# Kernel optimization log

Measured on AMD Instinct MI355X. Metric: run time of the kernel, lower is better.

Reference implementation:

```python
import jax, jax.numpy as jnp
import numpy as np

B, VL, TL, KL = 2, 2048, 448, 64  # batch, vision_len, text_len, task_len
H, NH, D = 1024, 16, 64           # hidden, num_heads, head_dim


def _linear(x, w, b):
    # torch nn.Linear convention: w is [out, in]
    return x @ w.T + b


def _attn(q, k, v):
    # q: [b, ql, n, d], k/v: [b, kl, n, d] -> [b, ql, n, d]
    d = q.shape[-1]
    scores = jnp.einsum('bqnd,bknd->bnqk', q, k) / d  # note: /d, not /sqrt(d), as in source
    probs = jax.nn.softmax(scores, axis=-1)
    return jnp.einsum('bnqk,bknd->bqnd', probs, v)


def setup_inputs() -> dict:
    key = jax.random.key(0)
    ks = jax.random.split(key, 20)
    s = 0.02
    inp = {
        'vision_hidden_states': jax.random.normal(ks[0], (B, VL, H), jnp.float32),
        'text_hidden_states': jax.random.normal(ks[1], (B, TL, H), jnp.float32),
        'task_hidden_states': jax.random.normal(ks[2], (B, KL, H), jnp.float32),
        'wq0': jax.random.normal(ks[3], (H, H), jnp.float32) * s,
        'bq0': jnp.zeros((H,), jnp.float32),
        'wk0': jax.random.normal(ks[4], (H, H), jnp.float32) * s,
        'bk0': jnp.zeros((H,), jnp.float32),
        'wv0': jax.random.normal(ks[5], (H, H), jnp.float32) * s,
        'bv0': jnp.zeros((H,), jnp.float32),
        'wq1': jax.random.normal(ks[6], (D, D), jnp.float32) * s,
        'bq1': jnp.zeros((D,), jnp.float32),
        'wk1': jax.random.normal(ks[7], (D, D), jnp.float32) * s,
        'bk1': jnp.zeros((D,), jnp.float32),
        'wv1': jax.random.normal(ks[8], (D, D), jnp.float32) * s,
        'bv1': jnp.zeros((D,), jnp.float32),
        'wo': jax.random.normal(ks[9], (H, H), jnp.float32) * s,
        'bo': jnp.zeros((H,), jnp.float32),
    }
    return inp


def reference(vision_hidden_states, text_hidden_states, task_hidden_states,
              wq0, bq0, wk0, bk0, wv0, bv0,
              wq1, bq1, wk1, bk1, wv1, bv1, wo, bo):
    b, vl, h = vision_hidden_states.shape
    tl = text_hidden_states.shape[1]
    kl = task_hidden_states.shape[1]
    total = vl + tl + kl

    hs = jnp.concatenate([vision_hidden_states, text_hidden_states, task_hidden_states], axis=1)
    q0 = _linear(hs, wq0, bq0).reshape(b, total, NH, D)
    k0 = _linear(hs, wk0, bk0).reshape(b, total, NH, D)
    v0 = _linear(hs, wv0, bv0).reshape(b, total, NH, D)

    vq, tq, kq = q0[:, :vl], q0[:, vl:vl + tl], q0[:, vl + tl:]
    vk, tk, kk = k0[:, :vl], k0[:, vl:vl + tl], k0[:, vl + tl:]
    vv, tv = v0[:, :vl], v0[:, vl:vl + tl]
    kv = q0[:, vl + tl:]  # faithful to source bug: task_v comes from q0

    v2t = _attn(vq, tk, tv)  # vision attends to text: [b, vl, n, d]
    t2v = _attn(tq, vk, vv)  # text attends to vision: [b, tl, n, d]
    mid = jnp.concatenate([v2t, t2v], axis=1)  # [b, vl+tl, n, d]

    q1 = jnp.concatenate([kq, _linear(mid, wq1, bq1)], axis=1)
    k1 = jnp.concatenate([kk, _linear(mid, wk1, bk1)], axis=1)
    v1 = jnp.concatenate([kv, _linear(mid, wv1, bv1)], axis=1)

    out = _attn(q1, k1, v1).reshape(b, total, NH * D)
    return _linear(out, wo, bo)
```

## Files before the change

kernel.cpp:

```cpp
#include <hip/hip_runtime.h>
#include <math.h>

#define NB   2
#define VL   2048
#define TL   448
#define KL   64
#define TOT  2560
#define MIDL 2496
#define HDIM 1024
#define NHEAD 16
#define DHEAD 64

typedef __bf16 bf16x8 __attribute__((ext_vector_type(8)));
typedef float  f32x4  __attribute__((ext_vector_type(4)));
typedef unsigned short us8 __attribute__((ext_vector_type(8)));
typedef float  fl4    __attribute__((ext_vector_type(4)));
typedef unsigned int u32x2 __attribute__((ext_vector_type(2)));

__device__ __forceinline__ unsigned short f2bf(float f) {
    unsigned int u = __builtin_bit_cast(unsigned int, f);
    u += 0x7FFFu + ((u >> 16) & 1u);
    return (unsigned short)(u >> 16);
}
__device__ __forceinline__ f32x4 mfma_bf16(bf16x8 a, bf16x8 b, f32x4 c) {
    return __builtin_amdgcn_mfma_f32_16x16x32_bf16(a, b, c, 0, 0, 0);
}
__device__ __forceinline__ bf16x8 ldb(const unsigned short* p) {
    return __builtin_bit_cast(bf16x8, *(const us8*)p);
}
__device__ __forceinline__ unsigned cvt_pk_bf16(float lo, float hi) {
    unsigned r;
    asm("v_cvt_pk_bf16_f32 %0, %1, %2" : "=v"(r) : "v"(lo), "v"(hi));
    return r;
}
__device__ __forceinline__ float exp2_fast(float x) {
    float r;
    asm("v_exp_f32 %0, %1" : "=v"(r) : "v"(x));
    return r;
}

__global__ __launch_bounds__(256) void k_cast_hs(
    const float* __restrict__ vis, const float* __restrict__ txt,
    const float* __restrict__ tsk, unsigned short* __restrict__ X)
{
    size_t idx = ((size_t)blockIdx.x * 256 + threadIdx.x) * 4;
    if (idx >= (size_t)NB * TOT * HDIM) return;
    size_t r = idx >> 10; int c = (int)(idx & 1023);
    int b = (int)(r / TOT), s = (int)(r % TOT);
    const float* src;
    if (s < VL)        src = vis + ((size_t)b * VL + s) * HDIM;
    else if (s < MIDL) src = txt + ((size_t)b * TL + (s - VL)) * HDIM;
    else               src = tsk + ((size_t)b * KL + (s - MIDL)) * HDIM;
    fl4 v = *(const fl4*)(src + c);
    X[idx + 0] = f2bf(v[0]); X[idx + 1] = f2bf(v[1]);
    X[idx + 2] = f2bf(v[2]); X[idx + 3] = f2bf(v[3]);
}

__global__ __launch_bounds__(256) void k_cast(
    const float* __restrict__ in, unsigned short* __restrict__ out, int n)
{
    int idx = (blockIdx.x * 256 + threadIdx.x) * 4;
    if (idx >= n) return;
    fl4 v = *(const fl4*)(in + idx);
    out[idx + 0] = f2bf(v[0]); out[idx + 1] = f2bf(v[1]);
    out[idx + 2] = f2bf(v[2]); out[idx + 3] = f2bf(v[3]);
}

template<bool BF16OUT>
__global__ __launch_bounds__(256) void k_gemm_bt(
    const unsigned short* __restrict__ A, const unsigned short* __restrict__ W,
    const float* __restrict__ bias, void* __restrict__ Cv,
    int M, int N, int K)
{
    __shared__ unsigned short As[128][40];
    __shared__ unsigned short Bs[128][40];
    const int row0 = blockIdx.x * 128, col0 = blockIdx.y * 128;
    const int t = threadIdx.x;
    const int lane = t & 63, wave = t >> 6;
    const int wr = wave >> 1, wc = wave & 1;
    const int lrow = lane & 15, lgrp = lane >> 4;

    f32x4 acc[4][4];
    #pragma unroll
    for (int m = 0; m < 4; ++m)
        #pragma unroll
        for (int n = 0; n < 4; ++n)
            acc[m][n] = (f32x4){0.f, 0.f, 0.f, 0.f};

    const int r = t >> 1, hc = (t & 1) * 16;
    const unsigned short* Ap = A + (size_t)(row0 + r) * K + hc;
    const unsigned short* Wp = W + (size_t)(col0 + r) * K + hc;

    for (int kk = 0; kk < K; kk += 32) {
        us8 a0 = *(const us8*)(Ap + kk);
        us8 a1 = *(const us8*)(Ap + kk + 8);
        us8 b0 = *(const us8*)(Wp + kk);
        us8 b1 = *(const us8*)(Wp + kk + 8);
        __syncthreads();
        *(us8*)&As[r][hc]     = a0;
        *(us8*)&As[r][hc + 8] = a1;
        *(us8*)&Bs[r][hc]     = b0;
        *(us8*)&Bs[r][hc + 8] = b1;
        __syncthreads();
        bf16x8 af[4], bfr[4];
        #pragma unroll
        for (int m = 0; m < 4; ++m) af[m]  = ldb(&As[wr*64 + m*16 + lrow][lgrp*8]);
        #pragma unroll
        for (int n = 0; n < 4; ++n) bfr[n] = ldb(&Bs[wc*64 + n*16 + lrow][lgrp*8]);
        #pragma unroll
        for (int m = 0; m < 4; ++m)
            #pragma unroll
            for (int n = 0; n < 4; ++n)
                acc[m][n] = mfma_bf16(af[m], bfr[n], acc[m][n]);
    }
    #pragma unroll
    for (int m = 0; m < 4; ++m) {
        #pragma unroll
        for (int n = 0; n < 4; ++n) {
            int col = col0 + wc*64 + n*16 + lrow;
            float bs = bias[col];
            #pragma unroll
            for (int q = 0; q < 4; ++q) {
                int row = row0 + wr*64 + m*16 + lgrp*4 + q;
                float v = acc[m][n][q] + bs;
                if (BF16OUT) ((unsigned short*)Cv)[(size_t)row * N + col] = f2bf(v);
                else         ((float*)Cv)[(size_t)row * N + col] = v;
            }
        }
    }
}

__global__ __launch_bounds__(256) void k_gemm_qkv(
    const unsigned short* __restrict__ A, const unsigned short* __restrict__ W,
    const float* __restrict__ b0, const float* __restrict__ b1,
    const float* __restrict__ b2,
    unsigned short* __restrict__ C0, unsigned short* __restrict__ C1,
    unsigned short* __restrict__ vT)
{
    __shared__ unsigned short As[128][40];
    __shared__ unsigned short Bs[128][40];
    const int row0 = blockIdx.x * 128, col0 = blockIdx.y * 128;
    const int t = threadIdx.x;
    const int lane = t & 63, wave = t >> 6;
    const int wr = wave >> 1, wc = wave & 1;
    const int lrow = lane & 15, lgrp = lane >> 4;

    f32x4 acc[4][4];
    #pragma unroll
    for (int m = 0; m < 4; ++m)
        #pragma unroll
        for (int n = 0; n < 4; ++n)
            acc[m][n] = (f32x4){0.f, 0.f, 0.f, 0.f};

    const int r = t >> 1, hc = (t & 1) * 16;
    const unsigned short* Ap = A + (size_t)(row0 + r) * HDIM + hc;
    const unsigned short* Wp = W + (size_t)(col0 + r) * HDIM + hc;

    for (int kk = 0; kk < HDIM; kk += 32) {
        us8 a0 = *(const us8*)(Ap + kk);
        us8 a1 = *(const us8*)(Ap + kk + 8);
        us8 b0v = *(const us8*)(Wp + kk);
        us8 b1v = *(const us8*)(Wp + kk + 8);
        __syncthreads();
        *(us8*)&As[r][hc]     = a0;
        *(us8*)&As[r][hc + 8] = a1;
        *(us8*)&Bs[r][hc]     = b0v;
        *(us8*)&Bs[r][hc + 8] = b1v;
        __syncthreads();
        bf16x8 af[4], bfr[4];
        #pragma unroll
        for (int m = 0; m < 4; ++m) af[m]  = ldb(&As[wr*64 + m*16 + lrow][lgrp*8]);
        #pragma unroll
        for (int n = 0; n < 4; ++n) bfr[n] = ldb(&Bs[wc*64 + n*16 + lrow][lgrp*8]);
        #pragma unroll
        for (int m = 0; m < 4; ++m)
            #pragma unroll
            for (int n = 0; n < 4; ++n)
                acc[m][n] = mfma_bf16(af[m], bfr[n], acc[m][n]);
    }
    const int plane = col0 >> 10;
    const int cl0 = col0 & 1023;
    if (plane < 2) {
        const float* bp = (plane == 0) ? b0 : b1;
        unsigned short* Cp = (plane == 0) ? C0 : C1;
        #pragma unroll
        for (int m = 0; m < 4; ++m)
            #pragma unroll
            for (int n = 0; n < 4; ++n) {
                int col = cl0 + wc*64 + n*16 + lrow;
                float bs = bp[col];
                #pragma unroll
                for (int q = 0; q < 4; ++q) {
                    int row = row0 + wr*64 + m*16 + lgrp*4 + q;
                    Cp[(size_t)row * HDIM + col] = f2bf(acc[m][n][q] + bs);
                }
            }
    } else {
        #pragma unroll
        for (int m = 0; m < 4; ++m)
            #pragma unroll
            for (int n = 0; n < 4; ++n) {
                int col = cl0 + wc*64 + n*16 + lrow;
                int hh = col >> 6, dd = col & 63;
                float bs = b2[col];
                int rowb = row0 + wr*64 + m*16 + lgrp*4;
                int bb = rowb / TOT, sq = rowb % TOT;
                u32x2 w;
                w[0] = cvt_pk_bf16(acc[m][n][0] + bs, acc[m][n][1] + bs);
                w[1] = cvt_pk_bf16(acc[m][n][2] + bs, acc[m][n][3] + bs);
                *(u32x2*)(vT + ((size_t)(bb*NHEAD + hh)*64 + dd)*TOT + sq) = w;
            }
    }
}

__global__ __launch_bounds__(256) void k_attn(
    const unsigned short* __restrict__ Qb, const unsigned short* __restrict__ Kb,
    const unsigned short* __restrict__ vT, unsigned short* __restrict__ Ob,
    int Lk, size_t q_bs, size_t k_bs, int v_seq0, size_t o_bs, float scale)
{
    __shared__ unsigned short QV[64 * 72];
    __shared__ unsigned short Ks[64][72];
    __shared__ unsigned short Pl[4][16][72];

    const int b = blockIdx.z, h = blockIdx.y, qb = blockIdx.x;
    const unsigned short* Q = Qb + (size_t)b * q_bs + h * 64;
    const unsigned short* K = Kb + (size_t)b * k_bs + h * 64;
    const unsigned short* V = vT + ((size_t)(b*NHEAD + h) * 64) * TOT + v_seq0;
    unsigned short*       O = Ob + (size_t)b * o_bs + h * 64;
    const int t = threadIdx.x;
    const int wave = t >> 6, lane = t & 63;
    const int lrow = lane & 15, lgrp = lane >> 4;
    const int q0r = qb * 64;

    #pragma unroll
    for (int i = 0; i < 2; ++i) {
        int c = t + i * 256, rr = c >> 3, off = (c & 7) * 8;
        *(us8*)&QV[rr*72 + off] = *(const us8*)(Q + (size_t)(q0r + rr) * HDIM + off);
    }
    __syncthreads();
    bf16x8 qf0 = ldb(&QV[(wave*16 + lrow)*72 + lgrp*8]);
    bf16x8 qf1 = ldb(&QV[(wave*16 + lrow)*72 + 32 + lgrp*8]);

    f32x4 oacc[4];
    #pragma unroll
    for (int d = 0; d < 4; ++d) oacc[d] = (f32x4){0.f, 0.f, 0.f, 0.f};
    float mr = -INFINITY;
    float lsum = 0.f;

    const int c0 = t,        rr0 = c0 >> 3, of0 = (c0 & 7) * 8;
    const int c1 = t + 256,  rr1 = c1 >> 3, of1 = (c1 & 7) * 8;
    const unsigned short* Kp0 = K + (size_t)rr0 * HDIM + of0;
    const unsigned short* Kp1 = K + (size_t)rr1 * HDIM + of1;
    const unsigned short* Vp0 = V + (size_t)rr0 * TOT + of0;
    const unsigned short* Vp1 = V + (size_t)rr1 * TOT + of1;

    const int nkt = Lk >> 6;
    us8 ka0 = *(const us8*)(Kp0);
    us8 ka1 = *(const us8*)(Kp1);
    us8 va0 = *(const us8*)(Vp0);
    us8 va1 = *(const us8*)(Vp1);

    for (int kt = 0; kt < nkt; ++kt) {
        __syncthreads();
        *(us8*)&Ks[rr0][of0] = ka0;
        *(us8*)&Ks[rr1][of1] = ka1;
        *(us8*)&QV[rr0*72 + of0] = va0;
        *(us8*)&QV[rr1*72 + of1] = va1;
        if (kt + 1 < nkt) {
            ka0 = *(const us8*)(Kp0 + (size_t)(kt+1) * 64 * HDIM);
            ka1 = *(const us8*)(Kp1 + (size_t)(kt+1) * 64 * HDIM);
            va0 = *(const us8*)(Vp0 + (kt+1) * 64);
            va1 = *(const us8*)(Vp1 + (kt+1) * 64);
        }
        __syncthreads();

        f32x4 s[4];
        #pragma unroll
        for (int nf = 0; nf < 4; ++nf) {
            bf16x8 kf0 = ldb(&Ks[nf*16 + lrow][lgrp*8]);
            bf16x8 kf1 = ldb(&Ks[nf*16 + lrow][32 + lgrp*8]);
            f32x4 z = (f32x4){0.f, 0.f, 0.f, 0.f};
            z = mfma_bf16(kf0, qf0, z);
            z = mfma_bf16(kf1, qf1, z);
            s[nf] = z * scale;
        }
        float mt = s[0][0];
        #pragma unroll
        for (int nf = 0; nf < 4; ++nf)
            #pragma unroll
            for (int rg = 0; rg < 4; ++rg)
                mt = fmaxf(mt, s[nf][rg]);
        mt = fmaxf(mt, __shfl_xor(mt, 16));
        mt = fmaxf(mt, __shfl_xor(mt, 32));
        if (!__all(mt <= mr + 8.f)) {
            float mnew = fmaxf(mr, mt);
            float al = exp2_fast(mr - mnew);
            mr = mnew;
            lsum *= al;
            #pragma unroll
            for (int d = 0; d < 4; ++d) oacc[d] *= al;
        }

        float rs = 0.f;
        #pragma unroll
        for (int nf = 0; nf < 4; ++nf) {
            float p0 = exp2_fast(s[nf][0] - mr);
            float p1 = exp2_fast(s[nf][1] - mr);
            float p2 = exp2_fast(s[nf][2] - mr);
            float p3 = exp2_fast(s[nf][3] - mr);
            rs += (p0 + p1) + (p2 + p3);
            u32x2 w;
            w[0] = cvt_pk_bf16(p0, p1);
            w[1] = cvt_pk_bf16(p2, p3);
            *(u32x2*)&Pl[wave][lrow][nf*16 + lgrp*4] = w;
        }
        rs += __shfl_xor(rs, 16);
        rs += __shfl_xor(rs, 32);
        lsum += rs;

        bf16x8 pb0 = ldb(&Pl[wave][lrow][lgrp*8]);
        bf16x8 pb1 = ldb(&Pl[wave][lrow][32 + lgrp*8]);
        #pragma unroll
        for (int df = 0; df < 4; ++df) {
            int d = df*16 + lrow;
            bf16x8 v0 = ldb(&QV[d*72 + lgrp*8]);
            bf16x8 v1 = ldb(&QV[d*72 + 32 + lgrp*8]);
            oacc[df] = mfma_bf16(v0, pb0, oacc[df]);
            oacc[df] = mfma_bf16(v1, pb1, oacc[df]);
        }
    }
    const float rcp = 1.0f / lsum;
    const int row = q0r + wave*16 + lrow;
    #pragma unroll
    for (int df = 0; df < 4; ++df) {
        u32x2 w;
        w[0] = cvt_pk_bf16(oacc[df][0] * rcp, oacc[df][1] * rcp);
        w[1] = cvt_pk_bf16(oacc[df][2] * rcp, oacc[df][3] * rcp);
        *(u32x2*)(O + (size_t)row * HDIM + df*16 + lgrp*4) = w;
    }
}

__global__ __launch_bounds__(256) void k_midlin(
    const unsigned short* __restrict__ mid,
    const unsigned short* __restrict__ wq, const unsigned short* __restrict__ wk,
    const unsigned short* __restrict__ wv,
    const float* __restrict__ bq, const float* __restrict__ bk,
    const float* __restrict__ bv,
    unsigned short* __restrict__ q1, unsigned short* __restrict__ k1,
    unsigned short* __restrict__ vT)
{
    __shared__ unsigned short As[128][72];
    const int r0 = blockIdx.x * 128, h = blockIdx.y;
    const int t = threadIdx.x;
    const int wave = t >> 6, lane = t & 63;
    const int lrow = lane & 15, lgrp = lane >> 4;

    #pragma unroll
    for (int i = 0; i < 4; ++i) {
        int c = t + i * 256, rr = c >> 3, off = (c & 7) * 8;
        *(us8*)&As[rr][off] = *(const us8*)(mid + (size_t)(r0 + rr) * HDIM + h*64 + off);
    }
    __syncthreads();
    bf16x8 af[2][2];
    #pragma unroll
    for (int m = 0; m < 2; ++m)
        #pragma unroll
        for (int kf = 0; kf < 2; ++kf)
            af[m][kf] = ldb(&As[wave*32 + m*16 + lrow][kf*32 + lgrp*8]);

    const unsigned short* ws[3] = {wq, wk, wv};
    const float* bs[3] = {bq, bk, bv};
    unsigned short* ds[2] = {q1, k1};
    #pragma unroll
    for (int o = 0; o < 3; ++o) {
        bf16x8 bfr[4][2];
        #pragma unroll
        for (int n = 0; n < 4; ++n)
            #pragma unroll
            for (int kf = 0; kf < 2; ++kf)
                bfr[n][kf] = __builtin_bit_cast(bf16x8,
                    *(const us8*)(ws[o] + (size_t)(n*16 + lrow) * 64 + kf*32 + lgrp*8));
        f32x4 acc[2][4];
        #pragma unroll
        for (int m = 0; m < 2; ++m)
            #pragma unroll
            for (int n = 0; n < 4; ++n) {
                f32x4 z = (f32x4){0.f, 0.f, 0.f, 0.f};
                z = mfma_bf16(af[m][0], bfr[n][0], z);
                z = mfma_bf16(af[m][1], bfr[n][1], z);
                acc[m][n] = z;
            }
        #pragma unroll
        for (int m = 0; m < 2; ++m)
            #pragma unroll
            for (int n = 0; n < 4; ++n) {
                float bb = bs[o][n*16 + lrow];
                if (o < 2) {
                    #pragma unroll
                    for (int q = 0; q < 4; ++q) {
                        int gr = r0 + wave*32 + m*16 + lgrp*4 + q;
                        int bi = gr / MIDL, sq = gr % MIDL;
                        size_t drow = (size_t)bi * TOT + 64 + sq;
                        ds[o][drow * HDIM + h*64 + n*16 + lrow] = f2bf(acc[m][n][q] + bb);
                    }
                } else {
                    int gr = r0 + wave*32 + m*16 + lgrp*4;
                    int bi = gr / MIDL, sq = gr % MIDL;
                    u32x2 w;
                    w[0] = cvt_pk_bf16(acc[m][n][0] + bb, acc[m][n][1] + bb);
                    w[1] = cvt_pk_bf16(acc[m][n][2] + bb, acc[m][n][3] + bb);
                    *(u32x2*)(vT + ((size_t)(bi*NHEAD + h)*64 + (n*16+lrow))*TOT
                              + 64 + sq) = w;
                }
            }
    }
}

__global__ __launch_bounds__(256) void k_copy_task(
    const unsigned short* __restrict__ q0, const unsigned short* __restrict__ k0,
    unsigned short* __restrict__ q1, unsigned short* __restrict__ k1,
    unsigned short* __restrict__ vT)
{
    int blk = blockIdx.x;
    int t = threadIdx.x;
    if (blk < 256) {
        int tensor = blk >> 7, rem = blk & 127;
        int b = rem >> 6, rr = rem & 63;
        const unsigned short* src = tensor ? k0 : q0;
        unsigned short* dst = tensor ? k1 : q1;
        size_t srow = (size_t)b * TOT + MIDL + rr;
        size_t drow = (size_t)b * TOT + rr;
        if (t < 128)
            ((us8*)(dst + drow * HDIM))[t] = ((const us8*)(src + srow * HDIM))[t];
    } else {
        int rem = blk - 256;
        int b = rem >> 4, h = rem & 15;
        const unsigned short* src = q0 + ((size_t)b * TOT + MIDL) * HDIM + h * 64;
        unsigned short* dst = vT + ((size_t)(b*NHEAD + h) * 64) * TOT;
        #pragma unroll
        for (int i = 0; i < 16; ++i) {
            int idx = t + i * 256;
            int r = idx & 63, d = idx >> 6;
            dst[(size_t)d * TOT + r] = src[(size_t)r * HDIM + d];
        }
    }
}

extern "C" void kernel_launch(void* const* d_in, const int* in_sizes, int n_in,
                              void* d_out, int out_size, void* d_ws, size_t ws_size,
                              hipStream_t stream)
{
    (void)in_sizes; (void)n_in; (void)out_size; (void)ws_size;
    const float* vis = (const float*)d_in[0];
    const float* txt = (const float*)d_in[1];
    const float* tsk = (const float*)d_in[2];
    const float* wq0 = (const float*)d_in[3];
    const float* bq0 = (const float*)d_in[4];
    const float* wk0 = (const float*)d_in[5];
    const float* bk0 = (const float*)d_in[6];
    const float* wv0 = (const float*)d_in[7];
    const float* bv0 = (const float*)d_in[8];
    const float* wq1 = (const float*)d_in[9];
    const float* bq1 = (const float*)d_in[10];
    const float* wk1 = (const float*)d_in[11];
    const float* bk1 = (const float*)d_in[12];
    const float* wv1 = (const float*)d_in[13];
    const float* bv1 = (const float*)d_in[14];
    const float* wo  = (const float*)d_in[15];
    const float* bo  = (const float*)d_in[16];

    char* ws = (char*)d_ws;
    size_t off = 0;
    auto carve = [&](size_t bytes) -> char* {
        char* p = ws + off;
        off += (bytes + 255) & ~(size_t)255;
        return p;
    };
    const size_t ELX = (size_t)NB * TOT * HDIM;
    unsigned short* X     = (unsigned short*)carve(ELX * 2);
    unsigned short* q0    = (unsigned short*)carve(ELX * 2);
    unsigned short* k0    = (unsigned short*)carve(ELX * 2);
    unsigned short* vT    = (unsigned short*)carve(ELX * 2);
    unsigned short* wqkvb = (unsigned short*)carve((size_t)3 * HDIM * HDIM * 2);
    unsigned short* wob   = (unsigned short*)carve((size_t)HDIM * HDIM * 2);
    unsigned short* wq1b  = (unsigned short*)carve(64 * 64 * 2);
    unsigned short* wk1b  = (unsigned short*)carve(64 * 64 * 2);
    unsigned short* wv1b  = (unsigned short*)carve(64 * 64 * 2);
    unsigned short* mid   = X;
    unsigned short* q1    = q0;
    unsigned short* k1    = k0;
    unsigned short* out2  = X;

    const float scale = 1.44269504088896341f / 64.0f;

    k_cast_hs<<<5120, 256, 0, stream>>>(vis, txt, tsk, X);
    k_cast<<<1024, 256, 0, stream>>>(wq0, wqkvb,                 HDIM * HDIM);
    k_cast<<<1024, 256, 0, stream>>>(wk0, wqkvb + 1024*1024,     HDIM * HDIM);
    k_cast<<<1024, 256, 0, stream>>>(wv0, wqkvb + 2*1024*1024,   HDIM * HDIM);
    k_cast<<<1024, 256, 0, stream>>>(wo,  wob,  HDIM * HDIM);
    k_cast<<<4, 256, 0, stream>>>(wq1, wq1b, 64 * 64);
    k_cast<<<4, 256, 0, stream>>>(wk1, wk1b, 64 * 64);
    k_cast<<<4, 256, 0, stream>>>(wv1, wv1b, 64 * 64);

    k_gemm_qkv<<<dim3(40, 24), 256, 0, stream>>>(
        X, wqkvb, bq0, bk0, bv0, q0, k0, vT);

    k_attn<<<dim3(VL/64, NHEAD, NB), 256, 0, stream>>>(
        q0, k0 + (size_t)VL * HDIM, vT, mid,
        TL, (size_t)TOT * HDIM, (size_t)TOT * HDIM, VL, (size_t)MIDL * HDIM, scale);
    k_attn<<<dim3(TL/64, NHEAD, NB), 256, 0, stream>>>(
        q0 + (size_t)VL * HDIM, k0, vT, mid + (size_t)VL * HDIM,
        VL, (size_t)TOT * HDIM, (size_t)TOT * HDIM, 0, (size_t)MIDL * HDIM, scale);

    k_copy_task<<<288, 256, 0, stream>>>(q0, k0, q1, k1, vT);
    k_midlin<<<dim3(39, NHEAD), 256, 0, stream>>>(
        mid, wq1b, wk1b, wv1b, bq1, bk1, bv1, q1, k1, vT);

    k_attn<<<dim3(TOT/64, NHEAD, NB), 256, 0, stream>>>(
        q1, k1, vT, out2,
        TOT, (size_t)TOT * HDIM, (size_t)TOT * HDIM, 0, (size_t)TOT * HDIM, scale);

    k_gemm_bt<false><<<dim3(40, 8), 256, 0, stream>>>(out2, wob, bo, (float*)d_out,
                                                      NB*TOT, HDIM, HDIM);
}
```

Before: 389.5 us.

## Use two waves per attention block, each handling 32 query rows

The attention kernel now runs 128 threads (2 waves) per 64-query block, and each wave processes two 16-row query fragments. Each K and V fragment read from LDS is therefore reused for two MFMAs, and fewer waves share the staging work. The softmax scaling is folded into an fma inside the exponent, with the lazy-rescale threshold adjusted to match. The trade-off is higher register pressure per thread and fewer waves per block to hide latency; launch bounds request 3 blocks per SIMD.

```diff
diff --git a/kernel.cpp b/kernel.cpp
--- a/kernel.cpp
+++ b/kernel.cpp
@@ -213,14 +213,14 @@
     }
 }
 
-__global__ __launch_bounds__(256) void k_attn(
+__global__ __launch_bounds__(128, 3) void k_attn(
     const unsigned short* __restrict__ Qb, const unsigned short* __restrict__ Kb,
     const unsigned short* __restrict__ vT, unsigned short* __restrict__ Ob,
-    int Lk, size_t q_bs, size_t k_bs, int v_seq0, size_t o_bs, float scale)
+    int Lk, size_t q_bs, size_t k_bs, int v_seq0, size_t o_bs, float sc)
 {
     __shared__ unsigned short QV[64 * 72];
     __shared__ unsigned short Ks[64][72];
-    __shared__ unsigned short Pl[4][16][72];
+    __shared__ unsigned short Pl[2][32][72];
 
     const int b = blockIdx.z, h = blockIdx.y, qb = blockIdx.x;
     const unsigned short* Q = Qb + (size_t)b * q_bs + h * 64;
@@ -228,115 +228,149 @@
     const unsigned short* V = vT + ((size_t)(b*NHEAD + h) * 64) * TOT + v_seq0;
     unsigned short*       O = Ob + (size_t)b * o_bs + h * 64;
     const int t = threadIdx.x;
-    const int wave = t >> 6, lane = t & 63;
+    const int w = t >> 6, lane = t & 63;
     const int lrow = lane & 15, lgrp = lane >> 4;
     const int q0r = qb * 64;
 
-    #pragma unroll
-    for (int i = 0; i < 2; ++i) {
-        int c = t + i * 256, rr = c >> 3, off = (c & 7) * 8;
-        *(us8*)&QV[rr*72 + off] = *(const us8*)(Q + (size_t)(q0r + rr) * HDIM + off);
-    }
+    const int srow = t >> 3, soff = (t & 7) * 8;
+    #pragma unroll
+    for (int i = 0; i < 4; ++i)
+        *(us8*)&QV[(srow + i*16)*72 + soff] =
+            *(const us8*)(Q + (size_t)(q0r + srow + i*16) * HDIM + soff);
     __syncthreads();
-    bf16x8 qf0 = ldb(&QV[(wave*16 + lrow)*72 + lgrp*8]);
-    bf16x8 qf1 = ldb(&QV[(wave*16 + lrow)*72 + 32 + lgrp*8]);
-
-    f32x4 oacc[4];
-    #pragma unroll
-    for (int d = 0; d < 4; ++d) oacc[d] = (f32x4){0.f, 0.f, 0.f, 0.f};
-    float mr = -INFINITY;
-    float lsum = 0.f;
-
-    const int c0 = t,        rr0 = c0 >> 3, of0 = (c0 & 7) * 8;
-    const int c1 = t + 256,  rr1 = c1 >> 3, of1 = (c1 & 7) * 8;
-    const unsigned short* Kp0 = K + (size_t)rr0 * HDIM + of0;
-    const unsigned short* Kp1 = K + (size_t)rr1 * HDIM + of1;
-    const unsigned short* Vp0 = V + (size_t)rr0 * TOT + of0;
-    const unsigned short* Vp1 = V + (size_t)rr1 * TOT + of1;
+    bf16x8 qf[2][2];
+    #pragma unroll
+    for (int qh = 0; qh < 2; ++qh) {
+        qf[qh][0] = ldb(&QV[(w*32 + qh*16 + lrow)*72 + lgrp*8]);
+        qf[qh][1] = ldb(&QV[(w*32 + qh*16 + lrow)*72 + 32 + lgrp*8]);
+    }
+
+    f32x4 oacc[2][4];
+    #pragma unroll
+    for (int qh = 0; qh < 2; ++qh)
+        #pragma unroll
+        for (int d = 0; d < 4; ++d) oacc[qh][d] = (f32x4){0.f, 0.f, 0.f, 0.f};
+    float mr0 = -INFINITY, mr1 = -INFINITY;
+    float ls0 = 0.f, ls1 = 0.f;
+    float msc0 = 0.f, msc1 = 0.f;
+    const float THRR = 8.0f / sc;
+
+    const unsigned short* Kp = K + (size_t)srow * HDIM + soff;
+    const unsigned short* Vp = V + (size_t)srow * TOT + soff;
 
     const int nkt = Lk >> 6;
-    us8 ka0 = *(const us8*)(Kp0);
-    us8 ka1 = *(const us8*)(Kp1);
-    us8 va0 = *(const us8*)(Vp0);
-    us8 va1 = *(const us8*)(Vp1);
+    us8 ka[4], va[4];
+    #pragma unroll
+    for (int i = 0; i < 4; ++i) {
+        ka[i] = *(const us8*)(Kp + (size_t)(i*16) * HDIM);
+        va[i] = *(const us8*)(Vp + (size_t)(i*16) * TOT);
+    }
 
     for (int kt = 0; kt < nkt; ++kt) {
         __syncthreads();
-        *(us8*)&Ks[rr0][of0] = ka0;
-        *(us8*)&Ks[rr1][of1] = ka1;
-        *(us8*)&QV[rr0*72 + of0] = va0;
-        *(us8*)&QV[rr1*72 + of1] = va1;
+        #pragma unroll
+        for (int i = 0; i < 4; ++i) {
+            *(us8*)&Ks[srow + i*16][soff] = ka[i];
+            *(us8*)&QV[(srow + i*16)*72 + soff] = va[i];
+        }
         if (kt + 1 < nkt) {
-            ka0 = *(const us8*)(Kp0 + (size_t)(kt+1) * 64 * HDIM);
-            ka1 = *(const us8*)(Kp1 + (size_t)(kt+1) * 64 * HDIM);
-            va0 = *(const us8*)(Vp0 + (kt+1) * 64);
-            va1 = *(const us8*)(Vp1 + (kt+1) * 64);
+            #pragma unroll
+            for (int i = 0; i < 4; ++i) {
+                ka[i] = *(const us8*)(Kp + (size_t)((kt+1)*64 + i*16) * HDIM);
+                va[i] = *(const us8*)(Vp + (size_t)(i*16) * TOT + (kt+1)*64);
+            }
         }
         __syncthreads();
 
-        f32x4 s[4];
+        f32x4 s[4][2];
         #pragma unroll
         for (int nf = 0; nf < 4; ++nf) {
             bf16x8 kf0 = ldb(&Ks[nf*16 + lrow][lgrp*8]);
             bf16x8 kf1 = ldb(&Ks[nf*16 + lrow][32 + lgrp*8]);
-            f32x4 z = (f32x4){0.f, 0.f, 0.f, 0.f};
-            z = mfma_bf16(kf0, qf0, z);
-            z = mfma_bf16(kf1, qf1, z);
-            s[nf] = z * scale;
-        }
-        float mt = s[0][0];
+            #pragma unroll
+            for (int qh = 0; qh < 2; ++qh) {
+                f32x4 z = (f32x4){0.f, 0.f, 0.f, 0.f};
+                z = mfma_bf16(kf0, qf[qh][0], z);
+                z = mfma_bf16(kf1, qf[qh][1], z);
+                s[nf][qh] = z;
+            }
+        }
+        float mt0 = s[0][0][0], mt1 = s[0][1][0];
         #pragma unroll
         for (int nf = 0; nf < 4; ++nf)
             #pragma unroll
-            for (int rg = 0; rg < 4; ++rg)
-                mt = fmaxf(mt, s[nf][rg]);
-        mt = fmaxf(mt, __shfl_xor(mt, 16));
-        mt = fmaxf(mt, __shfl_xor(mt, 32));
-        if (!__all(mt <= mr + 8.f)) {
-            float mnew = fmaxf(mr, mt);
-            float al = exp2_fast(mr - mnew);
-            mr = mnew;
-            lsum *= al;
-            #pragma unroll
-            for (int d = 0; d < 4; ++d) oacc[d] *= al;
-        }
-
-        float rs = 0.f;
+            for (int rg = 0; rg < 4; ++rg) {
+                mt0 = fmaxf(mt0, s[nf][0][rg]);
+                mt1 = fmaxf(mt1, s[nf][1][rg]);
+            }
+        mt0 = fmaxf(mt0, __shfl_xor(mt0, 16)); mt0 = fmaxf(mt0, __shfl_xor(mt0, 32));
+        mt1 = fmaxf(mt1, __shfl_xor(mt1, 16)); mt1 = fmaxf(mt1, __shfl_xor(mt1, 32));
+        if (!__all((mt0 - mr0 <= THRR) && (mt1 - mr1 <= THRR))) {
+            float n0 = fmaxf(mr0, mt0), n1 = fmaxf(mr1, mt1);
+            float a0 = exp2_fast(sc * (mr0 - n0));
+            float a1 = exp2_fast(sc * (mr1 - n1));
+            mr0 = n0; mr1 = n1; msc0 = sc * n0; msc1 = sc * n1;
+            ls0 *= a0; ls1 *= a1;
+            #pragma unroll
+            for (int d = 0; d < 4; ++d) { oacc[0][d] *= a0; oacc[1][d] *= a1; }
+        }
+
+        float rs0 = 0.f, rs1 = 0.f;
         #pragma unroll
         for (int nf = 0; nf < 4; ++nf) {
-            float p0 = exp2_fast(s[nf][0] - mr);
-            float p1 = exp2_fast(s[nf][1] - mr);
-            float p2 = exp2_fast(s[nf][2] - mr);
-            float p3 = exp2_fast(s[nf][3] - mr);
-            rs += (p0 + p1) + (p2 + p3);
-            u32x2 w;
-            w[0] = cvt_pk_bf16(p0, p1);
-            w[1] = cvt_pk_bf16(p2, p3);
-            *(u32x2*)&Pl[wave][lrow][nf*16 + lgrp*4] = w;
-        }
-        rs += __shfl_xor(rs, 16);
-        rs += __shfl_xor(rs, 32);
-        lsum += rs;
-
-        bf16x8 pb0 = ldb(&Pl[wave][lrow][lgrp*8]);
-        bf16x8 pb1 = ldb(&Pl[wave][lrow][32 + lgrp*8]);
+            float p00 = exp2_fast(fmaf(s[nf][0][0], sc, -msc0));
+            float p01 = exp2_fast(fmaf(s[nf][0][1], sc, -msc0));
+            float p02 = exp2_fast(fmaf(s[nf][0][2], sc, -msc0));
+            float p03 = exp2_fast(fmaf(s[nf][0][3], sc, -msc0));
+            rs0 += (p00 + p01) + (p02 + p03);
+            u32x2 w0;
+            w0[0] = cvt_pk_bf16(p00, p01);
+            w0[1] = cvt_pk_bf16(p02, p03);
+            *(u32x2*)&Pl[w][lrow][nf*16 + lgrp*4] = w0;
+            float p10 = exp2_fast(fmaf(s[nf][1][0], sc, -msc1));
+            float p11 = exp2_fast(fmaf(s[nf][1][1], sc, -msc1));
+            float p12 = exp2_fast(fmaf(s[nf][1][2], sc, -msc1));
+            float p13 = exp2_fast(fmaf(s[nf][1][3], sc, -msc1));
+            rs1 += (p10 + p11) + (p12 + p13);
+            u32x2 w1;
+            w1[0] = cvt_pk_bf16(p10, p11);
+            w1[1] = cvt_pk_bf16(p12, p13);
+            *(u32x2*)&Pl[w][16 + lrow][nf*16 + lgrp*4] = w1;
+        }
+        rs0 += __shfl_xor(rs0, 16); rs0 += __shfl_xor(rs0, 32);
+        rs1 += __shfl_xor(rs1, 16); rs1 += __shfl_xor(rs1, 32);
+        ls0 += rs0; ls1 += rs1;
+
+        bf16x8 pb[2][2];
+        #pragma unroll
+        for (int qh = 0; qh < 2; ++qh) {
+            pb[qh][0] = ldb(&Pl[w][qh*16 + lrow][lgrp*8]);
+            pb[qh][1] = ldb(&Pl[w][qh*16 + lrow][32 + lgrp*8]);
+        }
         #pragma unroll
         for (int df = 0; df < 4; ++df) {
             int d = df*16 + lrow;
             bf16x8 v0 = ldb(&QV[d*72 + lgrp*8]);
             bf16x8 v1 = ldb(&QV[d*72 + 32 + lgrp*8]);
-            oacc[df] = mfma_bf16(v0, pb0, oacc[df]);
-            oacc[df] = mfma_bf16(v1, pb1, oacc[df]);
-        }
-    }
-    const float rcp = 1.0f / lsum;
-    const int row = q0r + wave*16 + lrow;
-    #pragma unroll
-    for (int df = 0; df < 4; ++df) {
-        u32x2 w;
-        w[0] = cvt_pk_bf16(oacc[df][0] * rcp, oacc[df][1] * rcp);
-        w[1] = cvt_pk_bf16(oacc[df][2] * rcp, oacc[df][3] * rcp);
-        *(u32x2*)(O + (size_t)row * HDIM + df*16 + lgrp*4) = w;
+            #pragma unroll
+            for (int qh = 0; qh < 2; ++qh) {
+                oacc[qh][df] = mfma_bf16(v0, pb[qh][0], oacc[qh][df]);
+                oacc[qh][df] = mfma_bf16(v1, pb[qh][1], oacc[qh][df]);
+            }
+        }
+    }
+    const float rcp0 = 1.0f / ls0, rcp1 = 1.0f / ls1;
+    #pragma unroll
+    for (int qh = 0; qh < 2; ++qh) {
+        const float rcp = qh ? rcp1 : rcp0;
+        const int row = q0r + w*32 + qh*16 + lrow;
+        #pragma unroll
+        for (int df = 0; df < 4; ++df) {
+            u32x2 wv;
+            wv[0] = cvt_pk_bf16(oacc[qh][df][0] * rcp, oacc[qh][df][1] * rcp);
+            wv[1] = cvt_pk_bf16(oacc[qh][df][2] * rcp, oacc[qh][df][3] * rcp);
+            *(u32x2*)(O + (size_t)row * HDIM + df*16 + lgrp*4) = wv;
+        }
     }
 }
 
@@ -491,7 +525,7 @@
     unsigned short* k1    = k0;
     unsigned short* out2  = X;
 
-    const float scale = 1.44269504088896341f / 64.0f;
+    const float sc = 1.44269504088896341f / 64.0f;
 
     k_cast_hs<<<5120, 256, 0, stream>>>(vis, txt, tsk, X);
     k_cast<<<1024, 256, 0, stream>>>(wq0, wqkvb,                 HDIM * HDIM);
@@ -505,20 +539,20 @@
     k_gemm_qkv<<<dim3(40, 24), 256, 0, stream>>>(
         X, wqkvb, bq0, bk0, bv0, q0, k0, vT);
 
-    k_attn<<<dim3(VL/64, NHEAD, NB), 256, 0, stream>>>(
+    k_attn<<<dim3(VL/64, NHEAD, NB), 128, 0, stream>>>(
         q0, k0 + (size_t)VL * HDIM, vT, mid,
-        TL, (size_t)TOT * HDIM, (size_t)TOT * HDIM, VL, (size_t)MIDL * HDIM, scale);
-    k_attn<<<dim3(TL/64, NHEAD, NB), 256, 0, stream>>>(
+        TL, (size_t)TOT * HDIM, (size_t)TOT * HDIM, VL, (size_t)MIDL * HDIM, sc);
+    k_attn<<<dim3(TL/64, NHEAD, NB), 128, 0, stream>>>(
         q0 + (size_t)VL * HDIM, k0, vT, mid + (size_t)VL * HDIM,
-        VL, (size_t)TOT * HDIM, (size_t)TOT * HDIM, 0, (size_t)MIDL * HDIM, scale);
+        VL, (size_t)TOT * HDIM, (size_t)TOT * HDIM, 0, (size_t)MIDL * HDIM, sc);
 
     k_copy_task<<<288, 256, 0, stream>>>(q0, k0, q1, k1, vT);
     k_midlin<<<dim3(39, NHEAD), 256, 0, stream>>>(
         mid, wq1b, wk1b, wv1b, bq1, bk1, bv1, q1, k1, vT);
 
-    k_attn<<<dim3(TOT/64, NHEAD, NB), 256, 0, stream>>>(
+    k_attn<<<dim3(TOT/64, NHEAD, NB), 128, 0, stream>>>(
         q1, k1, vT, out2,
-        TOT, (size_t)TOT * HDIM, (size_t)TOT * HDIM, 0, (size_t)TOT * HDIM, scale);
+        TOT, (size_t)TOT * HDIM, (size_t)TOT * HDIM, 0, (size_t)TOT * HDIM, sc);
 
     k_gemm_bt<false><<<dim3(40, 8), 256, 0, stream>>>(out2, wob, bo, (float*)d_out,
                                                       NB*TOT, HDIM, HDIM);
```

Result: faster. 381.2 us (-2.1%).
